# Kernel optimization log

Hardware: AMD Instinct MI355X
Metric: run time of the kernel (lower is better)

## Reference

```python
import jax, jax.numpy as jnp
import numpy as np

B, N, K, F, OUT = 32, 2000, 32, 64, 128

def setup_inputs() -> dict:
    key = jax.random.key(0)
    k1, k2, k3, k4, k5 = jax.random.split(key, 5)
    x = jax.random.normal(k1, (B, N, F), dtype=jnp.float32)
    neighborhood = jax.random.randint(k2, (N, K), 0, N, dtype=jnp.int64)
    distances = jax.random.uniform(k3, (N, K), dtype=jnp.float32)
    # Linear(k*(F+1), OUT): torch default init scale ~ 1/sqrt(fan_in)
    fan_in = K * (F + 1)
    W = jax.random.normal(k4, (OUT, fan_in), dtype=jnp.float32) / np.sqrt(fan_in)
    b = jax.random.normal(k5, (OUT,), dtype=jnp.float32) / np.sqrt(fan_in)
    return {"x": x, "neighborhood": neighborhood, "distances": distances, "W": W, "b": b}

def reference(x, neighborhood, distances, W, b):
    batch, seq_len, feat = x.shape          # [B, N, F]
    k = neighborhood.shape[1]
    gathered = x[:, neighborhood, :]        # [B, N, K, F] gather over sequence dim
    d = jnp.broadcast_to(distances[None, :, :, None], (batch, seq_len, k, 1))
    h = jnp.concatenate([gathered, d], axis=-1)        # [B, N, K, F+1]
    h = h.reshape(batch, seq_len, k * (feat + 1))      # [B, N, K*(F+1)]
    out = jnp.einsum('bnf,of->bno', h, W) + b          # [B, N, OUT]
    return out
```

## Files before the change

### kernel.cpp

```cpp
#include <hip/hip_runtime.h>
#include <hip/hip_bf16.h>
#include <stdint.h>

typedef __attribute__((ext_vector_type(8)))  __bf16   bf16x8;
typedef __attribute__((ext_vector_type(16))) float    f32x16;
typedef __attribute__((ext_vector_type(8)))  float    f32x8;

#define NB   32
#define NN   2000
#define NK   32
#define NF   64
#define NOUT 128
#define NSTEP 130

#define GLOBAL_AS __attribute__((address_space(1)))
#define LDS_AS    __attribute__((address_space(3)))

__global__ void kprep(const float* __restrict__ x, const float* __restrict__ dist,
                      const float* __restrict__ W,
                      __bf16* __restrict__ xb2, __bf16* __restrict__ db,
                      __bf16* __restrict__ Wf) {
  const int t = threadIdx.x;
  if (blockIdx.x < NN) {
    const int n = blockIdx.x;
    const int col = t & 31, half = (t >> 5) & 1, s = t >> 6;
    const float* src = x + ((size_t)col * NN + n) * NF + s * 16 + half * 8;
    f32x8 v = *(const f32x8*)src;
    bf16x8 r;
#pragma unroll
    for (int j = 0; j < 8; ++j) r[j] = (__bf16)v[j];
    *(bf16x8*)((char*)xb2 + ((size_t)n << 12) + t * 16) = r;
    if (t < NK) db[n * NK + t] = (__bf16)dist[n * NK + t];
  } else {
    const int kstep = blockIdx.x - NN;
    const int lane = t & 63;
    const int wv = t >> 6;
    const int o = wv * 32 + (lane & 31);
    const int kbase = kstep * 16 + (lane >> 5) * 8;
    bf16x8 r;
#pragma unroll
    for (int j = 0; j < 8; ++j) {
      const int kg = kbase + j;
      const int c = (kg < 2048) ? ((kg >> 6) * 65 + (kg & 63)) : ((kg - 2048) * 65 + 64);
      r[j] = (__bf16)W[(size_t)o * 2080 + c];
    }
    *(bf16x8*)(Wf + (((size_t)kstep * 256 + t) << 3)) = r;
  }
}

__global__ __launch_bounds__(256, 2) void kmain(
    const int* __restrict__ nbrs, const float* __restrict__ bias,
    const __bf16* __restrict__ xb2, const __bf16* __restrict__ Wf,
    const __bf16* __restrict__ db, float* __restrict__ out) {
  __shared__ __align__(16) char lds[4][4][4096];

  const int n0   = blockIdx.x * 4;
  const int t    = threadIdx.x;
  const int lane = t & 63;
  const int w    = t >> 6;
  const int col  = lane & 31;
  const int half = lane >> 5;

  f32x16 acc0 = {}, acc1 = {}, acc2 = {}, acc3 = {};

  int myidx = 0;
  if (lane < NK) myidx = nbrs[(n0 + w) * NK + lane];

  const __bf16* wfp = Wf + (((size_t)(w * 64 + lane)) << 3);

  auto stage = [&](int buf, int c) {
    const int nb = __builtin_amdgcn_readlane(myidx, c);
    const char* g = (const char*)xb2 + ((size_t)nb << 12) + lane * 16;
    char* l = &lds[buf][w][0];
#pragma unroll
    for (int q = 0; q < 4; ++q)
      __builtin_amdgcn_global_load_lds(
          (const GLOBAL_AS uint32_t*)(g + (q << 10)),
          (LDS_AS uint32_t*)(l + (q << 10)), 16, 0, 0);
  };

  auto loadB = [&](bf16x8* B, int i) {
#pragma unroll
    for (int s = 0; s < 4; ++s)
      B[s] = *(const bf16x8*)(wfp + ((size_t)(i * 4 + s) << 11));
  };

  auto compute = [&](int buf, const bf16x8* B) {
#pragma unroll
    for (int s = 0; s < 4; ++s) {
      const char* lb = &lds[buf][0][0] + (s << 10) + lane * 16;
      bf16x8 a0 = *(const bf16x8*)(lb);
      bf16x8 a1 = *(const bf16x8*)(lb + 4096);
      bf16x8 a2 = *(const bf16x8*)(lb + 8192);
      bf16x8 a3 = *(const bf16x8*)(lb + 12288);
      acc0 = __builtin_amdgcn_mfma_f32_32x32x16_bf16(a0, B[s], acc0, 0, 0, 0);
      acc1 = __builtin_amdgcn_mfma_f32_32x32x16_bf16(a1, B[s], acc1, 0, 0, 0);
      acc2 = __builtin_amdgcn_mfma_f32_32x32x16_bf16(a2, B[s], acc2, 0, 0, 0);
      acc3 = __builtin_amdgcn_mfma_f32_32x32x16_bf16(a3, B[s], acc3, 0, 0, 0);
    }
  };

  bf16x8 BA[4], BB[4];

  stage(0, 0); stage(1, 1); stage(2, 2);
  loadB(BA, 0);

  for (int i = 0; i < 28; i += 2) {
    __builtin_amdgcn_s_barrier();
    stage((i + 3) & 3, i + 3);
    loadB(BB, i + 1);
    asm volatile("s_waitcnt vmcnt(8)" ::: "memory");
    __builtin_amdgcn_s_barrier();
    compute(i & 3, BA);

    __builtin_amdgcn_s_barrier();
    stage((i + 4) & 3, i + 4);
    loadB(BA, i + 2);
    asm volatile("s_waitcnt vmcnt(8)" ::: "memory");
    __builtin_amdgcn_s_barrier();
    compute((i + 1) & 3, BB);
  }
  __builtin_amdgcn_s_barrier();
  stage(31 & 3, 31);
  loadB(BB, 29);
  asm volatile("s_waitcnt vmcnt(8)" ::: "memory");
  __builtin_amdgcn_s_barrier();
  compute(28 & 3, BA);
  __builtin_amdgcn_s_barrier();
  loadB(BA, 30);
  asm volatile("s_waitcnt vmcnt(8)" ::: "memory");
  __builtin_amdgcn_s_barrier();
  compute(29 & 3, BB);
  __builtin_amdgcn_s_barrier();
  loadB(BB, 31);
  asm volatile("s_waitcnt vmcnt(4)" ::: "memory");
  __builtin_amdgcn_s_barrier();
  compute(30 & 3, BA);
  __builtin_amdgcn_s_barrier();
  asm volatile("s_waitcnt vmcnt(0)" ::: "memory");
  __builtin_amdgcn_s_barrier();
  compute(31 & 3, BB);

#pragma unroll
  for (int s = 0; s < 2; ++s) {
    bf16x8 bfr = *(const bf16x8*)(wfp + ((size_t)(128 + s) << 11));
    const char* dbase = (const char*)db + (size_t)n0 * 64 + s * 32 + half * 16;
    bf16x8 d0 = *(const bf16x8*)(dbase);
    bf16x8 d1 = *(const bf16x8*)(dbase + 64);
    bf16x8 d2 = *(const bf16x8*)(dbase + 128);
    bf16x8 d3 = *(const bf16x8*)(dbase + 192);
    acc0 = __builtin_amdgcn_mfma_f32_32x32x16_bf16(d0, bfr, acc0, 0, 0, 0);
    acc1 = __builtin_amdgcn_mfma_f32_32x32x16_bf16(d1, bfr, acc1, 0, 0, 0);
    acc2 = __builtin_amdgcn_mfma_f32_32x32x16_bf16(d2, bfr, acc2, 0, 0, 0);
    acc3 = __builtin_amdgcn_mfma_f32_32x32x16_bf16(d3, bfr, acc3, 0, 0, 0);
  }

  const int o = w * 32 + col;
  const float bv = bias[o];
#pragma unroll
  for (int r = 0; r < 16; ++r) {
    const int row = (r & 3) + 8 * (r >> 2) + 4 * half;
    float* op = out + ((size_t)row * NN + n0) * NOUT + o;
    op[0 * NOUT] = acc0[r] + bv;
    op[1 * NOUT] = acc1[r] + bv;
    op[2 * NOUT] = acc2[r] + bv;
    op[3 * NOUT] = acc3[r] + bv;
  }
}

extern "C" void kernel_launch(void* const* d_in, const int* in_sizes, int n_in,
                              void* d_out, int out_size, void* d_ws, size_t ws_size,
                              hipStream_t stream) {
  const float* x    = (const float*)d_in[0];
  const int*   nbrs = (const int*)d_in[1];
  const float* dist = (const float*)d_in[2];
  const float* W    = (const float*)d_in[3];
  const float* bias = (const float*)d_in[4];
  float* out = (float*)d_out;

  char* ws = (char*)d_ws;
  __bf16* xb2 = (__bf16*)(ws);
  __bf16* Wf  = (__bf16*)(ws + 8192000);
  __bf16* db  = (__bf16*)(ws + 8192000 + 532480);

  kprep<<<NN + NSTEP, 256, 0, stream>>>(x, dist, W, xb2, db, Wf);
  kmain<<<NN / 4, 256, 0, stream>>>(nbrs, bias, xb2, Wf, db, out);
}
```

Measured before the change: 55.25 us.

## Rework gather pipeline with one barrier per step, sched barriers and coalesced prep

The main loop is restructured so each compute step has a single barrier. It uses sched_barrier fences to pin the order of loads and MFMAs, and sets wave priority high during the MFMA blocks. The 4-deep LDS ring now keeps two stages in flight instead of three, and the vmcnt waits are adjusted to match. The prep kernel now reads x rows contiguously per batch and scatters them into the same swizzled bf16 layout, which makes its global reads coalesced. Less prefetch depth could expose gather latency, and the fixed instruction order removes freedom from the compiler's scheduler.

```diff
diff --git a/kernel.cpp b/kernel.cpp
--- a/kernel.cpp
+++ b/kernel.cpp
@@ -15,6 +15,7 @@
 
 #define GLOBAL_AS __attribute__((address_space(1)))
 #define LDS_AS    __attribute__((address_space(3)))
+#define SB() __builtin_amdgcn_sched_barrier(0)
 
 __global__ void kprep(const float* __restrict__ x, const float* __restrict__ dist,
                       const float* __restrict__ W,
@@ -23,13 +24,15 @@
   const int t = threadIdx.x;
   if (blockIdx.x < NN) {
     const int n = blockIdx.x;
-    const int col = t & 31, half = (t >> 5) & 1, s = t >> 6;
-    const float* src = x + ((size_t)col * NN + n) * NF + s * 16 + half * 8;
+    const int bb = t >> 3;
+    const int f0 = (t & 7) << 3;
+    const float* src = x + ((size_t)bb * NN + n) * NF + f0;
     f32x8 v = *(const f32x8*)src;
     bf16x8 r;
 #pragma unroll
     for (int j = 0; j < 8; ++j) r[j] = (__bf16)v[j];
-    *(bf16x8*)((char*)xb2 + ((size_t)n << 12) + t * 16) = r;
+    const int off = ((f0 >> 4) << 10) + (((f0 >> 3) & 1) << 9) + (bb << 4);
+    *(bf16x8*)((char*)xb2 + ((size_t)n << 12) + off) = r;
     if (t < NK) db[n * NK + t] = (__bf16)dist[n * NK + t];
   } else {
     const int kstep = blockIdx.x - NN;
@@ -86,6 +89,7 @@
   };
 
   auto compute = [&](int buf, const bf16x8* B) {
+    __builtin_amdgcn_s_setprio(1);
 #pragma unroll
     for (int s = 0; s < 4; ++s) {
       const char* lb = &lds[buf][0][0] + (s << 10) + lane * 16;
@@ -98,48 +102,34 @@
       acc2 = __builtin_amdgcn_mfma_f32_32x32x16_bf16(a2, B[s], acc2, 0, 0, 0);
       acc3 = __builtin_amdgcn_mfma_f32_32x32x16_bf16(a3, B[s], acc3, 0, 0, 0);
     }
+    __builtin_amdgcn_s_setprio(0);
   };
 
-  bf16x8 BA[4], BB[4];
+  bf16x8 B0[4], B1[4];
 
-  stage(0, 0); stage(1, 1); stage(2, 2);
-  loadB(BA, 0);
+  stage(0, 0); SB();
+  loadB(B0, 0); SB();
+  stage(1, 1); SB();
 
-  for (int i = 0; i < 28; i += 2) {
-    __builtin_amdgcn_s_barrier();
-    stage((i + 3) & 3, i + 3);
-    loadB(BB, i + 1);
-    asm volatile("s_waitcnt vmcnt(8)" ::: "memory");
-    __builtin_amdgcn_s_barrier();
-    compute(i & 3, BA);
-
-    __builtin_amdgcn_s_barrier();
-    stage((i + 4) & 3, i + 4);
-    loadB(BA, i + 2);
-    asm volatile("s_waitcnt vmcnt(8)" ::: "memory");
-    __builtin_amdgcn_s_barrier();
-    compute((i + 1) & 3, BB);
+  for (int j = 0; j < 30; j += 2) {
+    loadB(B1, j + 1); SB();
+    stage((j + 2) & 3, j + 2); SB();
+    asm volatile("s_waitcnt vmcnt(12)" ::: "memory");
+    __builtin_amdgcn_s_barrier(); SB();
+    compute(j & 3, B0);
+    loadB(B0, j + 2); SB();
+    stage((j + 3) & 3, j + 3); SB();
+    asm volatile("s_waitcnt vmcnt(12)" ::: "memory");
+    __builtin_amdgcn_s_barrier(); SB();
+    compute((j + 1) & 3, B1);
   }
-  __builtin_amdgcn_s_barrier();
-  stage(31 & 3, 31);
-  loadB(BB, 29);
+  loadB(B1, 31); SB();
   asm volatile("s_waitcnt vmcnt(8)" ::: "memory");
-  __builtin_amdgcn_s_barrier();
-  compute(28 & 3, BA);
-  __builtin_amdgcn_s_barrier();
-  loadB(BA, 30);
-  asm volatile("s_waitcnt vmcnt(8)" ::: "memory");
-  __builtin_amdgcn_s_barrier();
-  compute(29 & 3, BB);
-  __builtin_amdgcn_s_barrier();
-  loadB(BB, 31);
-  asm volatile("s_waitcnt vmcnt(4)" ::: "memory");
-  __builtin_amdgcn_s_barrier();
-  compute(30 & 3, BA);
-  __builtin_amdgcn_s_barrier();
+  __builtin_amdgcn_s_barrier(); SB();
+  compute(30 & 3, B0);
   asm volatile("s_waitcnt vmcnt(0)" ::: "memory");
-  __builtin_amdgcn_s_barrier();
-  compute(31 & 3, BB);
+  __builtin_amdgcn_s_barrier(); SB();
+  compute(31 & 3, B1);
 
 #pragma unroll
   for (int s = 0; s < 2; ++s) {
```

New measurement: 54.20 us. Within noise of the previous version (-1.9%).
